# Performance work log

Measured on AMD Instinct MI355X. Metric: run time of the kernel, lower is better.

Reference implementation:

```python
import jax, jax.numpy as jnp
import numpy as np

EPS = 1e-5
F_BIAS = 1.0
KEEP_H = 0.7
KEEP_C = 0.7


def _block_layernorm(x, gamma, beta, n_blocks, h):
    # Normalize each of the n_blocks chunks of width h independently,
    # then apply a single per-feature gain/bias of size n_blocks*h.
    B = x.shape[0]
    xb = x.reshape(B, n_blocks, h)
    mean = jnp.mean(xb, axis=-1, keepdims=True)
    var = jnp.mean(jnp.square(xb - mean), axis=-1, keepdims=True)
    xn = (xb - mean) * jax.lax.rsqrt(var + EPS)
    return xn.reshape(B, n_blocks * h) * gamma + beta


def setup_inputs() -> dict:
    key = jax.random.key(0)
    ks = jax.random.split(key, 7)
    B, X, H = 65536, 256, 256
    x = jax.random.normal(ks[0], (B, X), dtype=jnp.float32)
    h = jax.random.normal(ks[1], (B, H), dtype=jnp.float32)
    c = jax.random.normal(ks[2], (B, H), dtype=jnp.float32)
    # orthogonal-initializer stand-in: scaled gaussian
    W_full = jax.random.normal(ks[3], (X + H, 4 * H), dtype=jnp.float32) / np.sqrt(X + H)
    bias = jnp.zeros((4 * H,), dtype=jnp.float32)
    g1 = jnp.ones((4 * H,), dtype=jnp.float32)
    b1 = jnp.zeros((4 * H,), dtype=jnp.float32)
    g2 = jnp.ones((H,), dtype=jnp.float32)
    b2 = jnp.zeros((H,), dtype=jnp.float32)
    mask_h = jax.random.uniform(ks[4], (B, H), dtype=jnp.float32)
    mask_c = jax.random.uniform(ks[5], (B, H), dtype=jnp.float32)
    return {"x": x, "h": h, "c": c, "W_full": W_full, "bias": bias,
            "g1": g1, "b1": b1, "g2": g2, "b2": b2,
            "mask_h": mask_h, "mask_c": mask_c}


def reference(x, h, c, W_full, bias, g1, b1, g2, b2, mask_h, mask_c):
    H = h.shape[1]
    concat = jnp.concatenate([x, h], axis=1) @ W_full + bias       # [B, 4H]
    concat = _block_layernorm(concat, g1, b1, 4, H)
    i, j, f, o = jnp.split(concat, 4, axis=1)
    new_c = c * jax.nn.sigmoid(f + F_BIAS) + jax.nn.sigmoid(i) * jnp.tanh(j)
    new_c = _block_layernorm(new_c, g2, b2, 1, H)
    new_h = jnp.tanh(new_c) * jax.nn.sigmoid(o)
    # zoneout: keep the NEW state with prob keep, else carry over old state
    mh = (mask_h < KEEP_H).astype(new_h.dtype)
    mc = (mask_c < KEEP_C).astype(new_c.dtype)
    new_h = mh * new_h + (1.0 - mh) * h
    new_c = mc * new_c + (1.0 - mc) * c
    return (new_h, new_c)
```

## Files before the change

### kernel.cpp

```cpp
#include <hip/hip_runtime.h>


#define NTHREADS 512
#define TILE_M 64
#define PRE_STRIDE 20

typedef _Float16 half8 __attribute__((ext_vector_type(8)));
typedef _Float16 half4v __attribute__((ext_vector_type(4)));
typedef float float4v __attribute__((ext_vector_type(4)));

__device__ __forceinline__ float sigm(float x) {
  return __fdividef(1.0f, 1.0f + __expf(-x));
}
__device__ __forceinline__ float tanh_fast(float x) {
  return 2.0f * __fdividef(1.0f, 1.0f + __expf(-2.0f * x)) - 1.0f;
}
__device__ __forceinline__ void bar_lgkm() {
  asm volatile("s_waitcnt lgkmcnt(0)\ns_barrier" ::: "memory");
}

__global__ __launch_bounds__(256) void wt_kernel(const float* __restrict__ W,
                                                 _Float16* __restrict__ Wt) {
  __shared__ float tile[64][65];
  const int bn = blockIdx.x << 6;
  const int bk = blockIdx.y << 6;
  const int tid = threadIdx.x;
#pragma unroll
  for (int i = 0; i < 16; ++i) {
    int idx = (i << 8) + tid;
    int kk = idx >> 6, nn = idx & 63;
    tile[kk][nn] = W[(size_t)(bk + kk) * 1024 + bn + nn];
  }
  __syncthreads();
#pragma unroll
  for (int i = 0; i < 16; ++i) {
    int idx = (i << 8) + tid;
    int nn = idx >> 6, kk = idx & 63;
    Wt[(size_t)(bn + nn) * 512 + bk + kk] = (_Float16)tile[kk][nn];
  }
}

__global__ __launch_bounds__(NTHREADS, 2) void lstm_fused(
    const float* __restrict__ x, const float* __restrict__ hin,
    const float* __restrict__ cin, const _Float16* __restrict__ Wt,
    const float* __restrict__ bias, const float* __restrict__ g1,
    const float* __restrict__ b1, const float* __restrict__ g2,
    const float* __restrict__ b2, const float* __restrict__ mhp,
    const float* __restrict__ mcp, float* __restrict__ out) {
  extern __shared__ char smem[];
  _Float16* abuf = (_Float16*)smem;
  _Float16* preT = (_Float16*)smem;
  float* g1l = (float*)(smem + 40960);
  float* b1l = (float*)(smem + 45056);
  float* g2l = (float*)(smem + 49152);
  float* b2l = (float*)(smem + 50176);

  const int tid = threadIdx.x;
  const int wave = tid >> 6;
  const int lane = tid & 63;
  const int l15 = lane & 15;
  const int quad = lane >> 4;
  const int blockRow = blockIdx.x * TILE_M;

  g1l[tid] = g1[tid];
  g1l[tid + 512] = g1[tid + 512];
  b1l[tid] = b1[tid];
  b1l[tid + 512] = b1[tid + 512];
  if (tid < 256) {
    g2l[tid] = g2[tid];
    b2l[tid] = b2[tid];
  }

  float4v acc[4][8];
#pragma unroll
  for (int s = 0; s < 4; ++s)
#pragma unroll
    for (int c = 0; c < 8; ++c) acc[s][c] = (float4v){0.f, 0.f, 0.f, 0.f};

  const int arow = tid >> 3;
  const int ap4 = (tid & 7) << 2;
  const float* xrow = x + (size_t)(blockRow + arow) * 256 + ap4;
  const float* hrow = hin + (size_t)(blockRow + arow) * 256 + ap4;
  _Float16* adst =
      abuf + arow * 32 + (((ap4 >> 3) ^ ((arow ^ (arow >> 2)) & 3)) << 3) + (ap4 & 4);
  const int aslot = quad ^ ((l15 ^ (l15 >> 2)) & 3);

  const _Float16* wbase = Wt + ((size_t)(wave * 64 + l15) << 9) + (quad << 3);

  {
    float4 v = *(const float4*)xrow;
    *(half4v*)adst = (half4v){(_Float16)v.x, (_Float16)v.y, (_Float16)v.z, (_Float16)v.w};
  }
  half8 B0[4];
#pragma unroll
  for (int cc = 0; cc < 4; ++cc) B0[cc] = *(const half8*)(wbase + cc * 8192);
  float4 av1 = *(const float4*)(xrow + 32);
  bar_lgkm();

#pragma unroll 2
  for (int i = 0; i < 15; ++i) {
    float4 av2;
    if (i < 14) {
      const float* s2p = (i + 2 < 8) ? (xrow + (i + 2) * 32) : (hrow + (i - 6) * 32);
      av2 = *(const float4*)s2p;
    }
    half8 B1[4];
#pragma unroll
    for (int cc = 0; cc < 4; ++cc)
      B1[cc] = *(const half8*)(wbase + cc * 8192 + 262144 + i * 32);
    const _Float16* abr = abuf + ((i & 1) << 11);
    half8 af[4];
#pragma unroll
    for (int s = 0; s < 4; ++s)
      af[s] = *(const half8*)(abr + (s * 16 + l15) * 32 + aslot * 8);
    __builtin_amdgcn_s_setprio(1);
#pragma unroll
    for (int s = 0; s < 4; ++s)
#pragma unroll
      for (int cc = 0; cc < 4; ++cc)
        acc[s][cc] = __builtin_amdgcn_mfma_f32_16x16x32_f16(af[s], B0[cc], acc[s][cc], 0, 0, 0);
    __builtin_amdgcn_s_setprio(0);
    half8 B0n[4];
#pragma unroll
    for (int cc = 0; cc < 4; ++cc)
      B0n[cc] = *(const half8*)(wbase + cc * 8192 + (i + 1) * 32);
    __builtin_amdgcn_s_setprio(1);
#pragma unroll
    for (int s = 0; s < 4; ++s)
#pragma unroll
      for (int cc = 0; cc < 4; ++cc)
        acc[s][4 + cc] =
            __builtin_amdgcn_mfma_f32_16x16x32_f16(af[s], B1[cc], acc[s][4 + cc], 0, 0, 0);
    __builtin_amdgcn_s_setprio(0);
    {
      half4v hv = {(_Float16)av1.x, (_Float16)av1.y, (_Float16)av1.z, (_Float16)av1.w};
      *(half4v*)(adst + (((i + 1) & 1) << 11)) = hv;
    }
    if (i < 14) av1 = av2;
#pragma unroll
    for (int cc = 0; cc < 4; ++cc) B0[cc] = B0n[cc];
    bar_lgkm();
  }
  {
    half8 B1[4];
#pragma unroll
    for (int cc = 0; cc < 4; ++cc)
      B1[cc] = *(const half8*)(wbase + cc * 8192 + 262144 + 15 * 32);
    const _Float16* abr = abuf + ((15 & 1) << 11);
    half8 af[4];
#pragma unroll
    for (int s = 0; s < 4; ++s)
      af[s] = *(const half8*)(abr + (s * 16 + l15) * 32 + aslot * 8);
    __builtin_amdgcn_s_setprio(1);
#pragma unroll
    for (int s = 0; s < 4; ++s)
#pragma unroll
      for (int cc = 0; cc < 4; ++cc)
        acc[s][cc] = __builtin_amdgcn_mfma_f32_16x16x32_f16(af[s], B0[cc], acc[s][cc], 0, 0, 0);
#pragma unroll
    for (int s = 0; s < 4; ++s)
#pragma unroll
      for (int cc = 0; cc < 4; ++cc)
        acc[s][4 + cc] =
            __builtin_amdgcn_mfma_f32_16x16x32_f16(af[s], B1[cc], acc[s][4 + cc], 0, 0, 0);
    __builtin_amdgcn_s_setprio(0);
  }

  float* out_h = out;
  float* out_c = out + (size_t)65536 * 256;
  const int er = tid >> 5;
  const int et = tid & 31;
  const int ro = er ^ (((et >> 4) & 1) << 1);

#pragma unroll
  for (int p = 0; p < 4; ++p) {
    bar_lgkm();
#pragma unroll
    for (int c = 0; c < 8; ++c) {
      int n = ((c >> 2) << 9) + wave * 64 + ((c & 3) << 4) + l15;
      float bn = bias[n];
      float4v a = acc[p][c];
      _Float16 e0 = (_Float16)(a.x + bn), e1 = (_Float16)(a.y + bn);
      _Float16 e2 = (_Float16)(a.z + bn), e3 = (_Float16)(a.w + bn);
      half4v hv = (c & 1) ? (half4v){e2, e3, e0, e1} : (half4v){e0, e1, e2, e3};
      *(half4v*)(preT + n * PRE_STRIDE + (quad << 2)) = hv;
    }
    bar_lgkm();

    const int rg = blockRow + (p << 4) + er;
    float mean1[4], rstd1[4];
#pragma unroll
    for (int ch = 0; ch < 4; ++ch) {
      float s = 0.f, q = 0.f;
#pragma unroll
      for (int ss = 0; ss < 8; ++ss) {
        int n = (ch << 8) + (ss << 5) + et;
        float v = (float)preT[n * PRE_STRIDE + ro];
        s += v;
        q += v * v;
      }
#pragma unroll
      for (int m = 1; m < 32; m <<= 1) {
        s += __shfl_xor(s, m, 32);
        q += __shfl_xor(q, m, 32);
      }
      float mu = s * (1.0f / 256.0f);
      mean1[ch] = mu;
      rstd1[ch] = __frsqrt_rn(q * (1.0f / 256.0f) - mu * mu + 1e-5f);
    }

    float ncp[8], so[8], cv[8];
    float s2 = 0.f, q2 = 0.f;
#pragma unroll
    for (int ss = 0; ss < 8; ++ss) {
      int hc = (ss << 5) + et;
      float iv = ((float)preT[(hc)*PRE_STRIDE + ro] - mean1[0]) * rstd1[0] * g1l[hc] + b1l[hc];
      float jv = ((float)preT[(256 + hc) * PRE_STRIDE + ro] - mean1[1]) * rstd1[1] * g1l[256 + hc] + b1l[256 + hc];
      float fv = ((float)preT[(512 + hc) * PRE_STRIDE + ro] - mean1[2]) * rstd1[2] * g1l[512 + hc] + b1l[512 + hc];
      float ov = ((float)preT[(768 + hc) * PRE_STRIDE + ro] - mean1[3]) * rstd1[3] * g1l[768 + hc] + b1l[768 + hc];
      float cval = cin[(size_t)rg * 256 + hc];
      float nc = cval * sigm(fv + 1.0f) + sigm(iv) * tanh_fast(jv);
      ncp[ss] = nc;
      so[ss] = sigm(ov);
      cv[ss] = cval;
      s2 += nc;
      q2 += nc * nc;
    }
#pragma unroll
    for (int m = 1; m < 32; m <<= 1) {
      s2 += __shfl_xor(s2, m, 32);
      q2 += __shfl_xor(q2, m, 32);
    }
    float mu2 = s2 * (1.0f / 256.0f);
    float rstd2 = __frsqrt_rn(q2 * (1.0f / 256.0f) - mu2 * mu2 + 1e-5f);
#pragma unroll
    for (int ss = 0; ss < 8; ++ss) {
      int hc = (ss << 5) + et;
      size_t gi = (size_t)rg * 256 + hc;
      float ncn = (ncp[ss] - mu2) * rstd2 * g2l[hc] + b2l[hc];
      float nh = tanh_fast(ncn) * so[ss];
      float hval = hin[gi];
      out_h[gi] = (mhp[gi] < 0.7f) ? nh : hval;
      out_c[gi] = (mcp[gi] < 0.7f) ? ncn : cv[ss];
    }
  }
}

extern "C" void kernel_launch(void* const* d_in, const int* in_sizes, int n_in,
                              void* d_out, int out_size, void* d_ws, size_t ws_size,
                              hipStream_t stream) {
  (void)in_sizes; (void)n_in; (void)out_size; (void)ws_size;
  const float* x = (const float*)d_in[0];
  const float* h = (const float*)d_in[1];
  const float* c = (const float*)d_in[2];
  const float* W = (const float*)d_in[3];
  const float* bias = (const float*)d_in[4];
  const float* g1 = (const float*)d_in[5];
  const float* b1 = (const float*)d_in[6];
  const float* g2 = (const float*)d_in[7];
  const float* b2 = (const float*)d_in[8];
  const float* mh = (const float*)d_in[9];
  const float* mc = (const float*)d_in[10];
  _Float16* Wt = (_Float16*)d_ws;

  wt_kernel<<<dim3(16, 8), dim3(256), 0, stream>>>(W, Wt);
  lstm_fused<<<dim3(1024), dim3(NTHREADS), 51200, stream>>>(
      x, h, c, Wt, bias, g1, b1, g2, b2, mh, mc, (float*)d_out);
}
```

Before: 509.6 us.

## Stage weight tiles through LDS with async global-to-LDS loads

Weight fragments are no longer loaded from global memory into registers. They are now copied with global_load_lds into two swizzled LDS buffers, one for each gate half, and read back as MFMA operands, with vmcnt-aware barriers doing the double buffering. The activation tile drops to a single LDS buffer. The gamma/beta staging moves to after the GEMM because the second weight buffer overlaps that LDS region. The intent is to cut register pressure and let loads overlap compute, at the cost of more LDS traffic, a larger LDS allocation (69632 B per block) and extra barrier waits inside each iteration.

```diff
diff --git a/kernel.cpp b/kernel.cpp
--- a/kernel.cpp
+++ b/kernel.cpp
@@ -5,9 +5,18 @@
 #define TILE_M 64
 #define PRE_STRIDE 20
 
+#define BARRIER_VM(N) \
+  asm volatile("s_waitcnt vmcnt(" #N ") lgkmcnt(0)\ns_barrier" ::: "memory")
+
 typedef _Float16 half8 __attribute__((ext_vector_type(8)));
 typedef _Float16 half4v __attribute__((ext_vector_type(4)));
 typedef float float4v __attribute__((ext_vector_type(4)));
+
+__device__ __forceinline__ void async16(const void* g, void* l) {
+  __builtin_amdgcn_global_load_lds(
+      (const __attribute__((address_space(1))) unsigned int*)g,
+      (__attribute__((address_space(3))) unsigned int*)l, 16, 0, 0);
+}
 
 __device__ __forceinline__ float sigm(float x) {
   return __fdividef(1.0f, 1.0f + __expf(-x));
@@ -49,6 +58,8 @@
     const float* __restrict__ mcp, float* __restrict__ out) {
   extern __shared__ char smem[];
   _Float16* abuf = (_Float16*)smem;
+  _Float16* wTh0 = (_Float16*)(smem + 4096);
+  _Float16* wTh1 = (_Float16*)(smem + 36864);
   _Float16* preT = (_Float16*)smem;
   float* g1l = (float*)(smem + 40960);
   float* b1l = (float*)(smem + 45056);
@@ -61,15 +72,6 @@
   const int l15 = lane & 15;
   const int quad = lane >> 4;
   const int blockRow = blockIdx.x * TILE_M;
-
-  g1l[tid] = g1[tid];
-  g1l[tid + 512] = g1[tid + 512];
-  b1l[tid] = b1[tid];
-  b1l[tid + 512] = b1[tid + 512];
-  if (tid < 256) {
-    g2l[tid] = g2[tid];
-    b2l[tid] = b2[tid];
-  }
 
   float4v acc[4][8];
 #pragma unroll
@@ -85,85 +87,101 @@
       abuf + arow * 32 + (((ap4 >> 3) ^ ((arow ^ (arow >> 2)) & 3)) << 3) + (ap4 & 4);
   const int aslot = quad ^ ((l15 ^ (l15 >> 2)) & 3);
 
-  const _Float16* wbase = Wt + ((size_t)(wave * 64 + l15) << 9) + (quad << 3);
+  const int wnl0 = tid >> 2;
+  const int wj = (tid & 3) ^ ((wnl0 ^ (wnl0 >> 2)) & 3);
+  const char* wg = (const char*)Wt + (size_t)wnl0 * 1024 + wj * 16;
+  char* wl0 = (char*)wTh0 + tid * 16;
+  char* wl1 = (char*)wTh1 + tid * 16;
 
   {
     float4 v = *(const float4*)xrow;
     *(half4v*)adst = (half4v){(_Float16)v.x, (_Float16)v.y, (_Float16)v.z, (_Float16)v.w};
   }
-  half8 B0[4];
-#pragma unroll
-  for (int cc = 0; cc < 4; ++cc) B0[cc] = *(const half8*)(wbase + cc * 8192);
-  float4 av1 = *(const float4*)(xrow + 32);
-  bar_lgkm();
-
-#pragma unroll 2
+#pragma unroll
+  for (int it = 0; it < 4; ++it) async16(wg + it * 131072, wl0 + it * 8192);
+  BARRIER_VM(0);
+
   for (int i = 0; i < 15; ++i) {
-    float4 av2;
-    if (i < 14) {
-      const float* s2p = (i + 2 < 8) ? (xrow + (i + 2) * 32) : (hrow + (i - 6) * 32);
-      av2 = *(const float4*)s2p;
-    }
-    half8 B1[4];
-#pragma unroll
-    for (int cc = 0; cc < 4; ++cc)
-      B1[cc] = *(const half8*)(wbase + cc * 8192 + 262144 + i * 32);
-    const _Float16* abr = abuf + ((i & 1) << 11);
+#pragma unroll
+    for (int it = 0; it < 4; ++it)
+      async16(wg + 524288 + it * 131072 + i * 64, wl1 + it * 8192);
+    const float* sp = (i + 1 < 8) ? (xrow + (i + 1) * 32) : (hrow + (i - 7) * 32);
+    float4 av = *(const float4*)sp;
     half8 af[4];
 #pragma unroll
     for (int s = 0; s < 4; ++s)
-      af[s] = *(const half8*)(abr + (s * 16 + l15) * 32 + aslot * 8);
-    __builtin_amdgcn_s_setprio(1);
+      af[s] = *(const half8*)(abuf + (s * 16 + l15) * 32 + aslot * 8);
+    {
+      half8 bf[4];
+#pragma unroll
+      for (int cc = 0; cc < 4; ++cc)
+        bf[cc] = *(const half8*)(wTh0 + (wave * 64 + cc * 16 + l15) * 32 + aslot * 8);
+      __builtin_amdgcn_s_setprio(1);
+#pragma unroll
+      for (int s = 0; s < 4; ++s)
+#pragma unroll
+        for (int cc = 0; cc < 4; ++cc)
+          acc[s][cc] = __builtin_amdgcn_mfma_f32_16x16x32_f16(af[s], bf[cc], acc[s][cc], 0, 0, 0);
+      __builtin_amdgcn_s_setprio(0);
+    }
+    BARRIER_VM(1);
+
+#pragma unroll
+    for (int it = 0; it < 4; ++it)
+      async16(wg + it * 131072 + (i + 1) * 64, wl0 + it * 8192);
+    {
+      half8 bf[4];
+#pragma unroll
+      for (int cc = 0; cc < 4; ++cc)
+        bf[cc] = *(const half8*)(wTh1 + (wave * 64 + cc * 16 + l15) * 32 + aslot * 8);
+      __builtin_amdgcn_s_setprio(1);
+#pragma unroll
+      for (int s = 0; s < 4; ++s)
+#pragma unroll
+        for (int cc = 0; cc < 4; ++cc)
+          acc[s][4 + cc] =
+              __builtin_amdgcn_mfma_f32_16x16x32_f16(af[s], bf[cc], acc[s][4 + cc], 0, 0, 0);
+      __builtin_amdgcn_s_setprio(0);
+    }
+    *(half4v*)adst = (half4v){(_Float16)av.x, (_Float16)av.y, (_Float16)av.z, (_Float16)av.w};
+    BARRIER_VM(0);
+  }
+  {
+#pragma unroll
+    for (int it = 0; it < 4; ++it)
+      async16(wg + 524288 + it * 131072 + 15 * 64, wl1 + it * 8192);
+    half8 af[4];
 #pragma unroll
     for (int s = 0; s < 4; ++s)
-#pragma unroll
-      for (int cc = 0; cc < 4; ++cc)
-        acc[s][cc] = __builtin_amdgcn_mfma_f32_16x16x32_f16(af[s], B0[cc], acc[s][cc], 0, 0, 0);
-    __builtin_amdgcn_s_setprio(0);
-    half8 B0n[4];
-#pragma unroll
-    for (int cc = 0; cc < 4; ++cc)
-      B0n[cc] = *(const half8*)(wbase + cc * 8192 + (i + 1) * 32);
-    __builtin_amdgcn_s_setprio(1);
-#pragma unroll
-    for (int s = 0; s < 4; ++s)
-#pragma unroll
-      for (int cc = 0; cc < 4; ++cc)
-        acc[s][4 + cc] =
-            __builtin_amdgcn_mfma_f32_16x16x32_f16(af[s], B1[cc], acc[s][4 + cc], 0, 0, 0);
-    __builtin_amdgcn_s_setprio(0);
-    {
-      half4v hv = {(_Float16)av1.x, (_Float16)av1.y, (_Float16)av1.z, (_Float16)av1.w};
-      *(half4v*)(adst + (((i + 1) & 1) << 11)) = hv;
-    }
-    if (i < 14) av1 = av2;
-#pragma unroll
-    for (int cc = 0; cc < 4; ++cc) B0[cc] = B0n[cc];
-    bar_lgkm();
-  }
-  {
-    half8 B1[4];
-#pragma unroll
-    for (int cc = 0; cc < 4; ++cc)
-      B1[cc] = *(const half8*)(wbase + cc * 8192 + 262144 + 15 * 32);
-    const _Float16* abr = abuf + ((15 & 1) << 11);
-    half8 af[4];
-#pragma unroll
-    for (int s = 0; s < 4; ++s)
-      af[s] = *(const half8*)(abr + (s * 16 + l15) * 32 + aslot * 8);
-    __builtin_amdgcn_s_setprio(1);
-#pragma unroll
-    for (int s = 0; s < 4; ++s)
-#pragma unroll
-      for (int cc = 0; cc < 4; ++cc)
-        acc[s][cc] = __builtin_amdgcn_mfma_f32_16x16x32_f16(af[s], B0[cc], acc[s][cc], 0, 0, 0);
-#pragma unroll
-    for (int s = 0; s < 4; ++s)
-#pragma unroll
-      for (int cc = 0; cc < 4; ++cc)
-        acc[s][4 + cc] =
-            __builtin_amdgcn_mfma_f32_16x16x32_f16(af[s], B1[cc], acc[s][4 + cc], 0, 0, 0);
-    __builtin_amdgcn_s_setprio(0);
+      af[s] = *(const half8*)(abuf + (s * 16 + l15) * 32 + aslot * 8);
+    {
+      half8 bf[4];
+#pragma unroll
+      for (int cc = 0; cc < 4; ++cc)
+        bf[cc] = *(const half8*)(wTh0 + (wave * 64 + cc * 16 + l15) * 32 + aslot * 8);
+      __builtin_amdgcn_s_setprio(1);
+#pragma unroll
+      for (int s = 0; s < 4; ++s)
+#pragma unroll
+        for (int cc = 0; cc < 4; ++cc)
+          acc[s][cc] = __builtin_amdgcn_mfma_f32_16x16x32_f16(af[s], bf[cc], acc[s][cc], 0, 0, 0);
+      __builtin_amdgcn_s_setprio(0);
+    }
+    BARRIER_VM(0);
+    {
+      half8 bf[4];
+#pragma unroll
+      for (int cc = 0; cc < 4; ++cc)
+        bf[cc] = *(const half8*)(wTh1 + (wave * 64 + cc * 16 + l15) * 32 + aslot * 8);
+      __builtin_amdgcn_s_setprio(1);
+#pragma unroll
+      for (int s = 0; s < 4; ++s)
+#pragma unroll
+        for (int cc = 0; cc < 4; ++cc)
+          acc[s][4 + cc] =
+              __builtin_amdgcn_mfma_f32_16x16x32_f16(af[s], bf[cc], acc[s][4 + cc], 0, 0, 0);
+      __builtin_amdgcn_s_setprio(0);
+    }
   }
 
   float* out_h = out;
@@ -175,6 +193,16 @@
 #pragma unroll
   for (int p = 0; p < 4; ++p) {
     bar_lgkm();
+    if (p == 0) {
+      g1l[tid] = g1[tid];
+      g1l[tid + 512] = g1[tid + 512];
+      b1l[tid] = b1[tid];
+      b1l[tid + 512] = b1[tid + 512];
+      if (tid < 256) {
+        g2l[tid] = g2[tid];
+        b2l[tid] = b2[tid];
+      }
+    }
 #pragma unroll
     for (int c = 0; c < 8; ++c) {
       int n = ((c >> 2) << 9) + wave * 64 + ((c & 3) << 4) + l15;
@@ -264,6 +292,6 @@
   _Float16* Wt = (_Float16*)d_ws;
 
   wt_kernel<<<dim3(16, 8), dim3(256), 0, stream>>>(W, Wt);
-  lstm_fused<<<dim3(1024), dim3(NTHREADS), 51200, stream>>>(
+  lstm_fused<<<dim3(1024), dim3(NTHREADS), 69632, stream>>>(
       x, h, c, Wt, bias, g1, b1, g2, b2, mh, mc, (float*)d_out);
 }
```

New measurement: 485.1 us. -4.8%, faster.
